# Optimization experiments

Hardware: AMD Instinct MI355X
Metric: run time of the kernel (lower is better)

The kernel has to match this reference:

```python
import jax, jax.numpy as jnp
import numpy as np

EPS = 1e-12

def _l2norm(v, axis=-1):
    n = jnp.sqrt(jnp.sum(v * v, axis=axis, keepdims=True))
    return v / jnp.maximum(n, EPS)

def setup_inputs() -> dict:
    key = jax.random.key(0)
    ks = jax.random.split(key, 6)
    B, S, E, A = 256, 128, 768, 30
    x = jax.random.normal(ks[0], (B, S, E), dtype=jnp.float32)
    W_att = jax.random.normal(ks[1], (E, E), dtype=jnp.float32) * (1.0 / np.sqrt(E))
    b_att = jnp.zeros((E,), dtype=jnp.float32)
    W_red = jax.random.normal(ks[2], (E, A), dtype=jnp.float32) * (1.0 / np.sqrt(E))
    b_red = jnp.zeros((A,), dtype=jnp.float32)
    aspect_W = jax.random.normal(ks[3], (A, E), dtype=jnp.float32) * (1.0 / np.sqrt(E))
    # negatives: uniform over other batch elements (multinomial on ones - eye)
    idx = jax.random.randint(ks[4], (B, 10), 0, B - 1)
    neg_idx = (idx + (idx >= jnp.arange(B)[:, None])).astype(jnp.int32)  # skip self
    return {"x": x, "W_att": W_att, "b_att": b_att, "W_red": W_red,
            "b_red": b_red, "aspect_W": aspect_W, "neg_idx": neg_idx}

def reference(x, W_att, b_att, W_red, b_red, aspect_W, neg_idx):
    # --- LuongAttention(general): query = mean over seq ---
    q = x.mean(axis=1)                                   # [B,E]
    qW = q @ W_att + b_att                               # [B,E]
    scores = jnp.einsum('bse,be->bs', x, qW)             # [B,S]
    attn = jax.nn.softmax(scores, axis=-1)
    z_s = jnp.einsum('bs,bse->be', attn, x)              # attended sentence vec [B,E]
    # --- reduction + reconstruction ---
    composition = jax.nn.softmax(z_s @ W_red + b_red, axis=-1)  # [B,A]
    reconstructed = composition @ aspect_W                      # [B,E]
    # --- max-margin loss with gathered negatives ---
    r_s = _l2norm(reconstructed)                         # F.normalize
    z_n = z_s[neg_idx]                                   # [B,10,E] gather
    pos = jnp.einsum('be,be->b', z_s, r_s)[:, None]      # [B,1]
    negs = jnp.einsum('bne,be->bn', z_n, r_s)            # [B,10]
    J = 1.0 - pos + negs
    margin_loss = jnp.mean(jnp.maximum(J, 0.0))
    # --- orthogonal regularization on aspect embeddings ---
    T_n = _l2norm(aspect_W, axis=1)                      # [A,E]
    G = T_n @ T_n.T - jnp.eye(aspect_W.shape[0], dtype=aspect_W.dtype)
    reg = jnp.sqrt(jnp.sum(G * G))                       # Frobenius norm
    loss = reg + margin_loss
    return (z_s, reconstructed, loss)
```

## Files before the change

### kernel.cpp

```cpp
#include <hip/hip_runtime.h>
#include <hip/hip_bf16.h>
#include <math.h>

#define B 256
#define S 128
#define E 768
#define E4 192
#define NA 30
#define NNEG 10

#define K2_KC 96
#define K2_KR 192

__device__ __forceinline__ float dot4(float4 a, float4 b) {
    return a.x * b.x + a.y * b.y + a.z * b.z + a.w * b.w;
}
__device__ __forceinline__ float wave_reduce_sum(float v) {
#pragma unroll
    for (int off = 32; off; off >>= 1) v += __shfl_down(v, off);
    return v;
}
__device__ __forceinline__ float wave_reduce_max(float v) {
#pragma unroll
    for (int off = 32; off; off >>= 1) v = fmaxf(v, __shfl_down(v, off));
    return v;
}

__global__ __launch_bounds__(768) void mean_prep_kernel(const float* __restrict__ x,
                                                        const float* __restrict__ W_red,
                                                        const float* __restrict__ aspect_W,
                                                        float* __restrict__ q,
                                                        float* __restrict__ WredT,
                                                        float* __restrict__ invn) {
    int bid = blockIdx.x;
    int tid = threadIdx.x;
    __shared__ __align__(16) float4 part[4][E4];
    __shared__ float red[12];

    if (bid < 2 * B) {
        int b = bid >> 1, half = bid & 1;
        int c = tid % E4;
        int g = tid / E4;
        const float4* xb = (const float4*)(x + (size_t)b * S * E);
        int s0 = half * 64 + g * 16;
        float4 acc = make_float4(0.f, 0.f, 0.f, 0.f);
#pragma unroll 4
        for (int s = s0; s < s0 + 16; ++s) {
            float4 v = xb[(size_t)s * E4 + c];
            acc.x += v.x; acc.y += v.y; acc.z += v.z; acc.w += v.w;
        }
        part[g][c] = acc;
        __syncthreads();
        if (tid < E4) {
            float4 a0 = part[0][c], a1 = part[1][c], a2 = part[2][c], a3 = part[3][c];
            const float inv = 1.0f / (float)S;
            float4 r;
            r.x = (a0.x + a1.x + a2.x + a3.x) * inv;
            r.y = (a0.y + a1.y + a2.y + a3.y) * inv;
            r.z = (a0.z + a1.z + a2.z + a3.z) * inv;
            r.w = (a0.w + a1.w + a2.w + a3.w) * inv;
            ((float4*)q)[((size_t)half * B + b) * E4 + c] = r;
        }
    } else {
        int a = bid - 2 * B;
        WredT[(size_t)a * E + tid] = W_red[(size_t)tid * NA + a];
        int wave = tid >> 6, lane = tid & 63;
        float v = aspect_W[(size_t)a * E + tid];
        float ss = wave_reduce_sum(v * v);
        if (lane == 0) red[wave] = ss;
        __syncthreads();
        if (tid == 0) {
            float n = 0.f;
#pragma unroll
            for (int w = 0; w < 12; ++w) n += red[w];
            invn[a] = 1.0f / fmaxf(sqrtf(n), 1e-12f);
        }
    }
}

__global__ __launch_bounds__(256) void qw_partial_kernel(const float* __restrict__ q,
                                                         const float* __restrict__ W_att,
                                                         float* __restrict__ part) {
    int b0 = blockIdx.x * 64;
    int e0 = blockIdx.y * 64;
    int kz = blockIdx.z;
    int k0 = kz * K2_KR;
    int tid = threadIdx.x;

    __shared__ __align__(16) float qs[64][K2_KC + 4];
    __shared__ __align__(16) float ws[K2_KC][64];

    int r0 = (tid >> 3) * 2;
    int c0 = (tid & 7) * 8;

    float4 a00 = make_float4(0,0,0,0), a01 = make_float4(0,0,0,0);
    float4 a10 = make_float4(0,0,0,0), a11 = make_float4(0,0,0,0);

    for (int ch = 0; ch < 2; ++ch) {
        int kc0 = k0 + ch * K2_KC;
        {
            int row = tid >> 2, ks = (tid & 3) * 24;
            const float* src0 = q + (size_t)(b0 + row) * E + kc0 + ks;
            const float* src1 = src0 + (size_t)B * E;
#pragma unroll
            for (int j = 0; j < 6; ++j) {
                float4 v0 = *(const float4*)(src0 + 4 * j);
                float4 v1 = *(const float4*)(src1 + 4 * j);
                v0.x += v1.x; v0.y += v1.y; v0.z += v1.z; v0.w += v1.w;
                *(float4*)&qs[row][ks + 4 * j] = v0;
            }
        }
        for (int i = tid; i < K2_KC * 16; i += 256) {
            int row = i >> 4, e4 = (i & 15) * 4;
            *(float4*)&ws[row][e4] =
                *(const float4*)(W_att + (size_t)(kc0 + row) * E + e0 + e4);
        }
        __syncthreads();
#pragma unroll 4
        for (int k = 0; k < K2_KC; ++k) {
            float qa = qs[r0][k], qb = qs[r0 + 1][k];
            float4 w0 = *(const float4*)&ws[k][c0];
            float4 w1 = *(const float4*)&ws[k][c0 + 4];
            a00.x += qa * w0.x; a00.y += qa * w0.y; a00.z += qa * w0.z; a00.w += qa * w0.w;
            a01.x += qa * w1.x; a01.y += qa * w1.y; a01.z += qa * w1.z; a01.w += qa * w1.w;
            a10.x += qb * w0.x; a10.y += qb * w0.y; a10.z += qb * w0.z; a10.w += qb * w0.w;
            a11.x += qb * w1.x; a11.y += qb * w1.y; a11.z += qb * w1.z; a11.w += qb * w1.w;
        }
        __syncthreads();
    }
    float* dst = part + ((size_t)kz * B + b0 + r0) * E + e0 + c0;
    *(float4*)dst = a00; *(float4*)(dst + 4) = a01;
    *(float4*)(dst + E) = a10; *(float4*)(dst + E + 4) = a11;
}

__global__ __launch_bounds__(768) void attn_ortho_kernel(const float* __restrict__ x,
                                                         const float* __restrict__ part,
                                                         const float* __restrict__ b_att,
                                                         const float* __restrict__ aspect_W,
                                                         const float* __restrict__ invn,
                                                         float* __restrict__ z_s,
                                                         float* __restrict__ Gpart) {
    int bid = blockIdx.x;
    int tid = threadIdx.x, wave = tid >> 6, lane = tid & 63;
    __shared__ __align__(16) float4 qw4[E4];
    __shared__ float att[S];
    __shared__ float red[12];
    __shared__ __align__(16) float4 zpart[4][E4];

    if (bid >= B) {
        int i = bid - B;
        float inv_i = invn[i];
        if (tid < E4) {
            float4 v = ((const float4*)aspect_W)[(size_t)i * E4 + tid];
            v.x *= inv_i; v.y *= inv_i; v.z *= inv_i; v.w *= inv_i;
            qw4[tid] = v;
        }
        __syncthreads();
        float acc = 0.f;
        for (int j = wave; j < NA; j += 12) {
            const float4* aj = (const float4*)(aspect_W + (size_t)j * E);
            float d = 0.f;
#pragma unroll
            for (int jj = 0; jj < 3; ++jj)
                d += dot4(aj[lane + 64 * jj], qw4[lane + 64 * jj]);
            d = wave_reduce_sum(d);
            if (lane == 0) {
                float g = d * invn[j] - ((i == j) ? 1.f : 0.f);
                acc += g * g;
            }
        }
        if (lane == 0) red[wave] = acc;
        __syncthreads();
        if (tid == 0) {
            float s = 0.f;
#pragma unroll
            for (int w = 0; w < 12; ++w) s += red[w];
            Gpart[i] = s;
        }
        return;
    }

    int b = bid;
    const int N4 = B * E / 4;
    if (tid < E4) {
        const float4* p = (const float4*)part;
        size_t base = (size_t)b * E4 + tid;
        float4 s0 = p[base], s1 = p[base + N4], s2 = p[base + 2 * N4], s3 = p[base + 3 * N4];
        float4 bb = ((const float4*)b_att)[tid];
        float4 r;
        r.x = s0.x + s1.x + s2.x + s3.x + bb.x;
        r.y = s0.y + s1.y + s2.y + s3.y + bb.y;
        r.z = s0.z + s1.z + s2.z + s3.z + bb.z;
        r.w = s0.w + s1.w + s2.w + s3.w + bb.w;
        qw4[tid] = r;
    }
    __syncthreads();

    const float4* xb = (const float4*)(x + (size_t)b * S * E);

    for (int p2 = wave; p2 < S / 2; p2 += 12) {
        int sA = 2 * p2;
        const float4* rA = xb + (size_t)sA * E4;
        const float4* rB = rA + E4;
        float dA = 0.f, dB = 0.f;
#pragma unroll
        for (int j = 0; j < 3; ++j) {
            float4 qv = qw4[lane + 64 * j];
            dA += dot4(rA[lane + 64 * j], qv);
            dB += dot4(rB[lane + 64 * j], qv);
        }
#pragma unroll
        for (int off = 32; off; off >>= 1) {
            dA += __shfl_down(dA, off);
            dB += __shfl_down(dB, off);
        }
        if (lane == 0) { att[sA] = dA; att[sA + 1] = dB; }
    }
    __syncthreads();

    float v = (tid < S) ? att[tid] : -3.4e38f;
    if (tid < S) {
        float m = wave_reduce_max(v);
        if (lane == 0) red[wave] = m;
    }
    __syncthreads();
    float gm = fmaxf(red[0], red[1]);
    float ex = 0.f;
    if (tid < S) {
        ex = expf(v - gm);
        float ss = wave_reduce_sum(ex);
        if (lane == 0) red[4 + wave] = ss;
    }
    __syncthreads();
    float tot = red[4] + red[5];
    if (tid < S) att[tid] = ex / tot;
    __syncthreads();

    int c = tid % E4, g = tid / E4;
    float4 acc = make_float4(0.f, 0.f, 0.f, 0.f);
#pragma unroll 4
    for (int s = g * 32 + 31; s >= g * 32; --s) {
        float w = att[s];
        float4 xv = xb[(size_t)s * E4 + c];
        acc.x += w * xv.x; acc.y += w * xv.y; acc.z += w * xv.z; acc.w += w * xv.w;
    }
    zpart[g][c] = acc;
    __syncthreads();
    if (tid < E4) {
        float4 a0 = zpart[0][tid], a1 = zpart[1][tid], a2 = zpart[2][tid], a3 = zpart[3][tid];
        float4 r;
        r.x = a0.x + a1.x + a2.x + a3.x;
        r.y = a0.y + a1.y + a2.y + a3.y;
        r.z = a0.z + a1.z + a2.z + a3.z;
        r.w = a0.w + a1.w + a2.w + a3.w;
        ((float4*)z_s)[(size_t)b * E4 + tid] = r;
    }
}

__global__ __launch_bounds__(768) void recon_margin_kernel(const float* __restrict__ z_s,
                                                           const float* __restrict__ WredT,
                                                           const float* __restrict__ b_red,
                                                           const float* __restrict__ aspect_W,
                                                           const int* __restrict__ neg_idx,
                                                           float* __restrict__ recon,
                                                           float* __restrict__ mpart) {
    int b = blockIdx.x;
    int tid = threadIdx.x, wave = tid >> 6, lane = tid & 63;
    __shared__ __align__(16) float4 z4[E4];
    __shared__ float comp[NA];
    __shared__ __align__(16) float r_sh[E];
    __shared__ float red[12];
    __shared__ float dots[12];

    if (tid < E4) z4[tid] = ((const float4*)(z_s + (size_t)b * E))[tid];
    __syncthreads();

    for (int a = wave; a < NA; a += 12) {
        const float4* wr = (const float4*)(WredT + (size_t)a * E);
        float d = 0.f;
#pragma unroll
        for (int j = 0; j < 3; ++j)
            d += dot4(wr[lane + 64 * j], z4[lane + 64 * j]);
        d = wave_reduce_sum(d);
        if (lane == 0) comp[a] = d + b_red[a];
    }
    __syncthreads();

    if (wave == 0) {
        float v = (lane < NA) ? comp[lane] : -3.4e38f;
        float m = wave_reduce_max(v);
        m = __shfl(m, 0);
        float e = (lane < NA) ? expf(v - m) : 0.f;
        float ssum = wave_reduce_sum(e);
        ssum = __shfl(ssum, 0);
        if (lane < NA) comp[lane] = e / ssum;
    }
    __syncthreads();

    float r = 0.f;
    for (int a = 0; a < NA; ++a)
        r += comp[a] * aspect_W[(size_t)a * E + tid];
    recon[(size_t)b * E + tid] = r;
    r_sh[tid] = r;
    float sq = wave_reduce_sum(r * r);
    if (lane == 0) red[wave] = sq;
    __syncthreads();
    float tot = 0.f;
#pragma unroll
    for (int w = 0; w < 12; ++w) tot += red[w];
    float inv = 1.0f / fmaxf(sqrtf(tot), 1e-12f);

    if (wave <= NNEG) {
        int row = (wave == 0) ? b : neg_idx[b * NNEG + (wave - 1)];
        const float4* zr = (const float4*)(z_s + (size_t)row * E);
        const float4* rr = (const float4*)r_sh;
        float acc = 0.f;
#pragma unroll
        for (int j = 0; j < 3; ++j)
            acc += dot4(zr[lane + 64 * j], rr[lane + 64 * j]);
        acc = wave_reduce_sum(acc);
        if (lane == 0) dots[wave] = acc;
    }
    __syncthreads();
    if (tid == 0) {
        float pos = dots[0] * inv;
        float ssum = 0.f;
        for (int n = 1; n <= NNEG; ++n)
            ssum += fmaxf(1.f - pos + dots[n] * inv, 0.f);
        mpart[b] = ssum;
    }
}

__global__ __launch_bounds__(256) void loss_kernel(const float* __restrict__ Gpart,
                                                   const float* __restrict__ mpart,
                                                   float* __restrict__ loss_out) {
    int tid = threadIdx.x, wave = tid >> 6, lane = tid & 63;
    __shared__ float ra[4], rb[4];
    float fr = (tid < NA) ? Gpart[tid] : 0.f;
    fr = wave_reduce_sum(fr);
    if (lane == 0) ra[wave] = fr;
    float mp = mpart[tid];
    mp = wave_reduce_sum(mp);
    if (lane == 0) rb[wave] = mp;
    __syncthreads();
    if (tid == 0) {
        float frob = sqrtf(ra[0] + ra[1] + ra[2] + ra[3]);
        float msum = rb[0] + rb[1] + rb[2] + rb[3];
        loss_out[0] = frob + msum * (1.0f / (float)(B * NNEG));
    }
}

extern "C" void kernel_launch(void* const* d_in, const int* in_sizes, int n_in,
                              void* d_out, int out_size, void* d_ws, size_t ws_size,
                              hipStream_t stream) {
    const float* x        = (const float*)d_in[0];
    const float* W_att    = (const float*)d_in[1];
    const float* b_att    = (const float*)d_in[2];
    const float* W_red    = (const float*)d_in[3];
    const float* b_red    = (const float*)d_in[4];
    const float* aspect_W = (const float*)d_in[5];
    const int*   neg_idx  = (const int*)d_in[6];

    float* out   = (float*)d_out;
    float* z_s   = out;
    float* recon = out + (size_t)B * E;
    float* loss  = out + (size_t)2 * B * E;

    float* ws    = (float*)d_ws;
    float* q     = ws;
    float* part2 = q + (size_t)2 * B * E;
    float* WredT = part2 + (size_t)4 * B * E;
    float* invn  = WredT + (size_t)NA * E;
    float* Gpart = invn + 32;
    float* mpart = Gpart + 32;

    mean_prep_kernel<<<2 * B + NA, 768, 0, stream>>>(x, W_red, aspect_W, q, WredT, invn);
    qw_partial_kernel<<<dim3(4, 12, 4), 256, 0, stream>>>(q, W_att, part2);
    attn_ortho_kernel<<<B + NA, 768, 0, stream>>>(x, part2, b_att, aspect_W, invn, z_s, Gpart);
    recon_margin_kernel<<<B, 768, 0, stream>>>(z_s, WredT, b_red, aspect_W, neg_idx, recon, mpart);
    loss_kernel<<<1, 256, 0, stream>>>(Gpart, mpart, loss);
}
```

Measured before the change: 74.07 us.

## Split attention kernel into score and weighted-sum kernels with 2x block parallelism

The fused attention kernel becomes two kernels. A score kernel uses two blocks per batch, each computing half of the sequence scores and writing them to a workspace buffer. A z-vector kernel also uses two blocks per batch, each doing the softmax and then the weighted sum over one half of the embedding dimension. This doubles the block count so more of the GPU is busy, at the cost of an extra launch, a second read of x from global memory, and the softmax being recomputed in both z blocks.

```diff
diff --git a/kernel.cpp b/kernel.cpp
--- a/kernel.cpp
+++ b/kernel.cpp
@@ -133,22 +133,20 @@
     *(float4*)(dst + E) = a10; *(float4*)(dst + E + 4) = a11;
 }
 
-__global__ __launch_bounds__(768) void attn_ortho_kernel(const float* __restrict__ x,
-                                                         const float* __restrict__ part,
-                                                         const float* __restrict__ b_att,
-                                                         const float* __restrict__ aspect_W,
-                                                         const float* __restrict__ invn,
-                                                         float* __restrict__ z_s,
-                                                         float* __restrict__ Gpart) {
+__global__ __launch_bounds__(768) void score_ortho_kernel(const float* __restrict__ x,
+                                                          const float* __restrict__ part,
+                                                          const float* __restrict__ b_att,
+                                                          const float* __restrict__ aspect_W,
+                                                          const float* __restrict__ invn,
+                                                          float* __restrict__ sc,
+                                                          float* __restrict__ Gpart) {
     int bid = blockIdx.x;
     int tid = threadIdx.x, wave = tid >> 6, lane = tid & 63;
     __shared__ __align__(16) float4 qw4[E4];
-    __shared__ float att[S];
     __shared__ float red[12];
-    __shared__ __align__(16) float4 zpart[4][E4];
-
-    if (bid >= B) {
-        int i = bid - B;
+
+    if (bid >= 2 * B) {
+        int i = bid - 2 * B;
         float inv_i = invn[i];
         if (tid < E4) {
             float4 v = ((const float4*)aspect_W)[(size_t)i * E4 + tid];
@@ -180,7 +178,7 @@
         return;
     }
 
-    int b = bid;
+    int b = bid >> 1, h = bid & 1;
     const int N4 = B * E / 4;
     if (tid < E4) {
         const float4* p = (const float4*)part;
@@ -197,9 +195,8 @@
     __syncthreads();
 
     const float4* xb = (const float4*)(x + (size_t)b * S * E);
-
-    for (int p2 = wave; p2 < S / 2; p2 += 12) {
-        int sA = 2 * p2;
+    for (int p2 = wave; p2 < 32; p2 += 12) {
+        int sA = h * 64 + 2 * p2;
         const float4* rA = xb + (size_t)sA * E4;
         const float4* rB = rA + E4;
         float dA = 0.f, dB = 0.f;
@@ -214,11 +211,21 @@
             dA += __shfl_down(dA, off);
             dB += __shfl_down(dB, off);
         }
-        if (lane == 0) { att[sA] = dA; att[sA + 1] = dB; }
-    }
-    __syncthreads();
-
-    float v = (tid < S) ? att[tid] : -3.4e38f;
+        if (lane == 0) { sc[b * S + sA] = dA; sc[b * S + sA + 1] = dB; }
+    }
+}
+
+__global__ __launch_bounds__(768) void zvec_kernel(const float* __restrict__ x,
+                                                   const float* __restrict__ sc,
+                                                   float* __restrict__ z_s) {
+    int bid = blockIdx.x;
+    int b = bid >> 1, eh = bid & 1;
+    int tid = threadIdx.x, wave = tid >> 6, lane = tid & 63;
+    __shared__ float att[S];
+    __shared__ float red[8];
+    __shared__ __align__(16) float4 zpart[8][96];
+
+    float v = (tid < S) ? sc[b * S + tid] : -3.4e38f;
     if (tid < S) {
         float m = wave_reduce_max(v);
         if (lane == 0) red[wave] = m;
@@ -236,24 +243,26 @@
     if (tid < S) att[tid] = ex / tot;
     __syncthreads();
 
-    int c = tid % E4, g = tid / E4;
+    int c = tid % 96;
+    int g = tid / 96;
+    const float4* xb = (const float4*)(x + (size_t)b * S * E) + eh * 96;
     float4 acc = make_float4(0.f, 0.f, 0.f, 0.f);
 #pragma unroll 4
-    for (int s = g * 32 + 31; s >= g * 32; --s) {
+    for (int s = g * 16; s < g * 16 + 16; ++s) {
         float w = att[s];
         float4 xv = xb[(size_t)s * E4 + c];
         acc.x += w * xv.x; acc.y += w * xv.y; acc.z += w * xv.z; acc.w += w * xv.w;
     }
     zpart[g][c] = acc;
     __syncthreads();
-    if (tid < E4) {
-        float4 a0 = zpart[0][tid], a1 = zpart[1][tid], a2 = zpart[2][tid], a3 = zpart[3][tid];
-        float4 r;
-        r.x = a0.x + a1.x + a2.x + a3.x;
-        r.y = a0.y + a1.y + a2.y + a3.y;
-        r.z = a0.z + a1.z + a2.z + a3.z;
-        r.w = a0.w + a1.w + a2.w + a3.w;
-        ((float4*)z_s)[(size_t)b * E4 + tid] = r;
+    if (tid < 96) {
+        float4 r = make_float4(0.f, 0.f, 0.f, 0.f);
+#pragma unroll
+        for (int gg = 0; gg < 8; ++gg) {
+            float4 a = zpart[gg][tid];
+            r.x += a.x; r.y += a.y; r.z += a.z; r.w += a.w;
+        }
+        ((float4*)z_s)[(size_t)b * E4 + eh * 96 + tid] = r;
     }
 }
 
@@ -373,10 +382,12 @@
     float* invn  = WredT + (size_t)NA * E;
     float* Gpart = invn + 32;
     float* mpart = Gpart + 32;
+    float* sc    = mpart + B;
 
     mean_prep_kernel<<<2 * B + NA, 768, 0, stream>>>(x, W_red, aspect_W, q, WredT, invn);
     qw_partial_kernel<<<dim3(4, 12, 4), 256, 0, stream>>>(q, W_att, part2);
-    attn_ortho_kernel<<<B + NA, 768, 0, stream>>>(x, part2, b_att, aspect_W, invn, z_s, Gpart);
+    score_ortho_kernel<<<2 * B + NA, 768, 0, stream>>>(x, part2, b_att, aspect_W, invn, sc, Gpart);
+    zvec_kernel<<<2 * B, 768, 0, stream>>>(x, sc, z_s);
     recon_margin_kernel<<<B, 768, 0, stream>>>(z_s, WredT, b_red, aspect_W, neg_idx, recon, mpart);
     loss_kernel<<<1, 256, 0, stream>>>(Gpart, mpart, loss);
 }
```

Result: slower. 79.11 us (+6.8%).
